# Optimization experiments

Hardware: AMD Instinct MI355X
Metric: run time of the kernel (lower is better)

The kernel has to match this reference:

```python
import jax, jax.numpy as jnp
import numpy as np

N_NODES = 50000
N_EDGES = 800000
IN_DIM = 128
HID_DIM = 128
OUT_DIM = 128
NUM_GRAPHS = 64
NUM_CLASSES = 3


def _glorot(key, shape):
    lim = np.sqrt(6.0 / (shape[0] + shape[1])).astype(np.float32)
    return jax.random.uniform(key, shape, jnp.float32, -lim, lim)


def setup_inputs() -> dict:
    key = jax.random.key(0)
    ks = jax.random.split(key, 10)
    x = jax.random.normal(ks[0], (N_NODES, IN_DIM), jnp.float32)
    edge_index = jax.random.randint(ks[1], (2, N_EDGES), 0, N_NODES, jnp.int32).astype(jnp.int64)
    batch = jnp.sort(jax.random.randint(ks[2], (N_NODES,), 0, NUM_GRAPHS, jnp.int32)).astype(jnp.int64)
    return {
        "x": x,
        "edge_index": edge_index,
        "batch": batch,
        "W1": _glorot(ks[3], (IN_DIM, HID_DIM)),  "b1": jnp.zeros((HID_DIM,), jnp.float32),
        "W2": _glorot(ks[4], (HID_DIM, HID_DIM)), "b2": jnp.zeros((HID_DIM,), jnp.float32),
        "W3": _glorot(ks[5], (HID_DIM, OUT_DIM)), "b3": jnp.zeros((OUT_DIM,), jnp.float32),
        "C1": _glorot(ks[6], (OUT_DIM, HID_DIM)), "bc1": jnp.zeros((HID_DIM,), jnp.float32),
        "C2": _glorot(ks[7], (HID_DIM, NUM_CLASSES)), "bc2": jnp.zeros((NUM_CLASSES,), jnp.float32),
    }


def _gcn_conv(x, src, dst, norm, W, b):
    # PyG GCNConv: linear transform, then normalized gather/scatter aggregation, then bias.
    h = x @ W                               # [N, F_out]
    msg = h[src] * norm[:, None]            # [E+N, F_out] irregular gather
    return jax.ops.segment_sum(msg, dst, num_segments=N_NODES) + b


def reference(x, edge_index, batch, W1, b1, W2, b2, W3, b3, C1, bc1, C2, bc2):
    loops = jnp.arange(N_NODES, dtype=edge_index.dtype)
    src = jnp.concatenate([edge_index[0], loops])  # add self-loops as in GCNConv
    dst = jnp.concatenate([edge_index[1], loops])
    deg = jax.ops.segment_sum(jnp.ones_like(dst, jnp.float32), dst, num_segments=N_NODES)
    dinv = jnp.where(deg > 0, jax.lax.rsqrt(deg), 0.0)
    norm = dinv[src] * dinv[dst]            # symmetric D^-1/2 (A+I) D^-1/2 weights

    # dropout(p=0.2) is identity at inference time
    h = jax.nn.relu(_gcn_conv(x, src, dst, norm, W1, b1))
    h = jax.nn.relu(_gcn_conv(h, src, dst, norm, W2, b2))
    h = _gcn_conv(h, src, dst, norm, W3, b3)

    # global mean pool over batch segment ids
    counts = jax.ops.segment_sum(jnp.ones((N_NODES,), jnp.float32), batch, num_segments=NUM_GRAPHS)
    pooled = jax.ops.segment_sum(h, batch, num_segments=NUM_GRAPHS) / jnp.maximum(counts, 1.0)[:, None]

    g = jax.nn.relu(pooled @ C1 + bc1)      # classifier MLP (dropout 0.3 inactive)
    return g @ C2 + bc2                     # [NUM_GRAPHS, 3]
```

## Files before the change

### kernel.cpp

```cpp
#include <hip/hip_runtime.h>
#include <hip/hip_bf16.h>

#define N_NODES    50000
#define DIM        128
#define NUM_GRAPHS 64
#define NUM_CLASSES 3
#define NPAD       50176
#define XPITCH     136

typedef unsigned short ushort_t;
typedef unsigned int   uint_t;
typedef __attribute__((ext_vector_type(8))) short short8;
typedef __attribute__((ext_vector_type(4))) float f32x4;

__device__ __forceinline__ ushort_t f2bf(float f) {
    union { float f; uint_t u; } v; v.f = f;
    uint_t r = v.u + 0x7fffu + ((v.u >> 16) & 1u);
    return (ushort_t)(r >> 16);
}
__device__ __forceinline__ float bflo(uint_t u) {
    union { uint_t u; float f; } v; v.u = u << 16; return v.f;
}
__device__ __forceinline__ float bfhi(uint_t u) {
    union { uint_t u; float f; } v; v.u = u & 0xffff0000u; return v.f;
}

__device__ __forceinline__ void gather_raw(
    int n, int lane, const int* __restrict__ rowptr,
    const int* __restrict__ csr_src, const uint_t* __restrict__ Tb,
    float2& acc)
{
    int p0 = rowptr[n], p1 = rowptr[n + 1];
    uint_t us = Tb[n * 64 + lane];
    float2 a0 = make_float2(bflo(us), bfhi(us));
    float2 a1 = make_float2(0.f, 0.f);
    int p = p0;
    int nb = (p1 - p0) >> 3;
    if (nb > 0) {
        uint_t ucur[8];
        #pragma unroll
        for (int q = 0; q < 8; ++q) ucur[q] = Tb[csr_src[p + q] * 64 + lane];
        for (int b = 1; b < nb; ++b) {
            uint_t unxt[8];
            #pragma unroll
            for (int q = 0; q < 8; ++q) unxt[q] = Tb[csr_src[p + 8 + q] * 64 + lane];
            #pragma unroll
            for (int q = 0; q < 8; q += 2) {
                a0.x += bflo(ucur[q]);     a0.y += bfhi(ucur[q]);
                a1.x += bflo(ucur[q + 1]); a1.y += bfhi(ucur[q + 1]);
            }
            #pragma unroll
            for (int q = 0; q < 8; ++q) ucur[q] = unxt[q];
            p += 8;
        }
        #pragma unroll
        for (int q = 0; q < 8; q += 2) {
            a0.x += bflo(ucur[q]);     a0.y += bfhi(ucur[q]);
            a1.x += bflo(ucur[q + 1]); a1.y += bfhi(ucur[q + 1]);
        }
        p += 8;
    }
    for (; p + 4 <= p1; p += 4) {
        int s[4]; uint_t u[4];
        #pragma unroll
        for (int q = 0; q < 4; ++q) s[q] = csr_src[p + q];
        #pragma unroll
        for (int q = 0; q < 4; ++q) u[q] = Tb[s[q] * 64 + lane];
        #pragma unroll
        for (int q = 0; q < 4; q += 2) {
            a0.x += bflo(u[q]);     a0.y += bfhi(u[q]);
            a1.x += bflo(u[q + 1]); a1.y += bfhi(u[q + 1]);
        }
    }
    for (; p < p1; ++p) {
        int s = csr_src[p];
        uint_t u = Tb[s * 64 + lane];
        a0.x += bflo(u); a0.y += bfhi(u);
    }
    acc.x += a0.x + a1.x;
    acc.y += a0.y + a1.y;
}

__global__ void k_init(int* degi, float* pooled, float* counts) {
    int i = blockIdx.x * 256 + threadIdx.x;
    if (i < NPAD) degi[i] = 0;
    if (i < NUM_GRAPHS * DIM) pooled[i] = 0.0f;
    if (i < NUM_GRAPHS) counts[i] = 0.0f;
}

__global__ void k_prep(const float* __restrict__ W1, const float* __restrict__ W2,
                       const float* __restrict__ W3, ushort_t* __restrict__ Wt) {
    int i = blockIdx.x * 256 + threadIdx.x;
    int mat = i >> 14;
    int idx = i & 16383;
    const float* W = (mat == 0) ? W1 : (mat == 1) ? W2 : W3;
    int n = idx >> 7, k = idx & 127;
    Wt[mat * 16384 + n * 128 + k] = f2bf(W[k * 128 + n]);
}

__global__ void k_count(const int* __restrict__ dst, int* degi, int* rank, int nedges) {
    int e = blockIdx.x * 256 + threadIdx.x;
    if (e < nedges) rank[e] = atomicAdd(&degi[dst[e]], 1);
}

__global__ __launch_bounds__(256) void k_scan1(const int* __restrict__ degi,
                                               int* rowptr, int* bsum) {
    __shared__ int sh[256];
    int i = blockIdx.x * 256 + threadIdx.x;
    int v = degi[i];
    sh[threadIdx.x] = v;
    __syncthreads();
    for (int off = 1; off < 256; off <<= 1) {
        int t = (threadIdx.x >= off) ? sh[threadIdx.x - off] : 0;
        __syncthreads();
        sh[threadIdx.x] += t;
        __syncthreads();
    }
    rowptr[i] = sh[threadIdx.x] - v;
    if (threadIdx.x == 255) bsum[blockIdx.x] = sh[255];
}

__global__ __launch_bounds__(256) void k_scan2(int* bsum, int nblocks) {
    __shared__ int sh[256];
    int v = (threadIdx.x < nblocks) ? bsum[threadIdx.x] : 0;
    sh[threadIdx.x] = v;
    __syncthreads();
    for (int off = 1; off < 256; off <<= 1) {
        int t = (threadIdx.x >= off) ? sh[threadIdx.x - off] : 0;
        __syncthreads();
        sh[threadIdx.x] += t;
        __syncthreads();
    }
    if (threadIdx.x < nblocks) bsum[threadIdx.x] = sh[threadIdx.x] - v;
}

__global__ __launch_bounds__(256) void k_scan3(int* rowptr, const int* __restrict__ bsum,
                                               const int* __restrict__ degi,
                                               float* dinv) {
    int i = blockIdx.x * 256 + threadIdx.x;
    rowptr[i] = rowptr[i] + bsum[blockIdx.x];
    if (i < N_NODES) dinv[i] = rsqrtf((float)degi[i] + 1.0f);
}

__global__ void k_fill(const int* __restrict__ src, const int* __restrict__ dst,
                       const int* __restrict__ rank, const int* __restrict__ rowptr,
                       int* csr_src, int nedges) {
    int e = blockIdx.x * 256 + threadIdx.x;
    if (e < nedges) csr_src[rowptr[dst[e]] + rank[e]] = src[e];
}

__global__ __launch_bounds__(256) void k_mm1(
    const float* __restrict__ xin, const ushort_t* __restrict__ WtG,
    const float* __restrict__ dinv, ushort_t* __restrict__ TbOut)
{
    __shared__ ushort_t Wl[DIM * XPITCH];
    __shared__ ushort_t Xl[64 * XPITCH];

    const int tid = threadIdx.x;
    const int rowbase = blockIdx.x * 64;

    #pragma unroll
    for (int i = 0; i < 8; ++i) {
        int g = tid + i * 256;
        uint4 v = ((const uint4*)WtG)[g];
        *((uint4*)&Wl[(g >> 4) * XPITCH + (g & 15) * 8]) = v;
    }
    #pragma unroll
    for (int i = 0; i < 8; ++i) {
        int c = tid + i * 256;
        int row = c >> 5;
        int grow = rowbase + row;
        float4 f = make_float4(0.f, 0.f, 0.f, 0.f);
        if (grow < N_NODES)
            f = ((const float4*)xin)[(long long)rowbase * 32 + c];
        ushort4 h;
        h.x = f2bf(f.x); h.y = f2bf(f.y); h.z = f2bf(f.z); h.w = f2bf(f.w);
        *((ushort4*)&Xl[row * XPITCH + (c & 31) * 4]) = h;
    }
    __syncthreads();

    const int wave = tid >> 6;
    const int lane = tid & 63;
    const int quad = lane >> 4;
    const int lm   = lane & 15;
    const int m0   = wave * 16;

    short8 af[4];
    #pragma unroll
    for (int k0 = 0; k0 < 4; ++k0)
        af[k0] = *(const short8*)&Xl[(m0 + lm) * XPITCH + k0 * 32 + quad * 8];

    int noder[4]; float di[4]; bool okr[4];
    #pragma unroll
    for (int r = 0; r < 4; ++r) {
        noder[r] = rowbase + m0 + quad * 4 + r;
        okr[r] = (noder[r] < N_NODES);
        di[r] = okr[r] ? dinv[noder[r]] : 0.f;
    }

    for (int n0 = 0; n0 < DIM; n0 += 16) {
        f32x4 acc = {0.f, 0.f, 0.f, 0.f};
        #pragma unroll
        for (int k0 = 0; k0 < 4; ++k0) {
            short8 bf = *(const short8*)&Wl[(n0 + lm) * XPITCH + k0 * 32 + quad * 8];
            acc = __builtin_amdgcn_mfma_f32_16x16x32_bf16(af[k0], bf, acc, 0, 0, 0);
        }
        int n = n0 + lm;
        #pragma unroll
        for (int r = 0; r < 4; ++r)
            if (okr[r])
                TbOut[(long long)noder[r] * DIM + n] = f2bf(acc[r] * di[r]);
    }
}

__global__ __launch_bounds__(256) void k_fused(
    const int* __restrict__ rowptr, const int* __restrict__ csr_src,
    const float* __restrict__ dinv, const uint_t* __restrict__ TbIn,
    const ushort_t* __restrict__ WtG, const float* __restrict__ b_prev,
    ushort_t* __restrict__ TbOut)
{
    __shared__ ushort_t Xl[16 * XPITCH];

    const int tid = threadIdx.x;
    const int rowbase = blockIdx.x * 16;
    const int wave = tid >> 6;
    const int lane = tid & 63;

    float2 bias2 = ((const float2*)b_prev)[lane];

    #pragma unroll
    for (int t = 0; t < 4; ++t) {
        int r = wave * 4 + t;
        int n = rowbase + r;
        float2 acc = make_float2(0.f, 0.f);
        float dd = 0.f;
        if (n < N_NODES) {
            dd = dinv[n];
            gather_raw(n, lane, rowptr, csr_src, TbIn, acc);
        }
        ushort2 h;
        h.x = f2bf(fmaxf(bias2.x + acc.x * dd, 0.f));
        h.y = f2bf(fmaxf(bias2.y + acc.y * dd, 0.f));
        *((ushort2*)&Xl[r * XPITCH + lane * 2]) = h;
    }
    __syncthreads();

    const int quad = lane >> 4;
    const int lm   = lane & 15;

    short8 af[4];
    #pragma unroll
    for (int k0 = 0; k0 < 4; ++k0)
        af[k0] = *(const short8*)&Xl[lm * XPITCH + k0 * 32 + quad * 8];

    int noder[4]; float di[4]; bool okr[4];
    #pragma unroll
    for (int r = 0; r < 4; ++r) {
        noder[r] = rowbase + quad * 4 + r;
        okr[r] = (noder[r] < N_NODES);
        di[r] = okr[r] ? dinv[noder[r]] : 0.f;
    }

    #pragma unroll
    for (int h = 0; h < 2; ++h) {
        int n0 = wave * 32 + h * 16;
        f32x4 acc = {0.f, 0.f, 0.f, 0.f};
        #pragma unroll
        for (int k0 = 0; k0 < 4; ++k0) {
            short8 bf = *(const short8*)&WtG[(n0 + lm) * DIM + k0 * 32 + quad * 8];
            acc = __builtin_amdgcn_mfma_f32_16x16x32_bf16(af[k0], bf, acc, 0, 0, 0);
        }
        int n = n0 + lm;
        #pragma unroll
        for (int r = 0; r < 4; ++r)
            if (okr[r])
                TbOut[(long long)noder[r] * DIM + n] = f2bf(acc[r] * di[r]);
    }
}

__global__ __launch_bounds__(256) void k_poolgather(
    const int* __restrict__ rowptr, const int* __restrict__ csr_src,
    const float* __restrict__ dinv, const uint_t* __restrict__ Tb,
    const float* __restrict__ b3, const int* __restrict__ batch,
    float* pooled, float* counts)
{
    __shared__ float lp[8][DIM];
    __shared__ float lc[8];

    const int tid  = threadIdx.x;
    const int wave = tid >> 6;
    const int lane = tid & 63;
    const int blk0 = blockIdx.x * 32;

    #pragma unroll
    for (int i = 0; i < 4; ++i) ((float*)lp)[tid + i * 256] = 0.f;
    if (tid < 8) lc[tid] = 0.f;
    __syncthreads();

    const int gbase = batch[min(blk0, N_NODES - 1)];
    int n0 = blk0 + wave * 8;

    if (n0 < N_NODES) {
        int nend = min(n0 + 8, N_NODES);
        float2 bias2 = ((const float2*)b3)[lane];
        int cur = batch[n0];
        int runstart = n0;
        float2 pacc = make_float2(0.f, 0.f);

        for (int n = n0; n < nend; ++n) {
            int g = batch[n];
            if (g != cur) {
                int slot = cur - gbase;
                if (slot < 8) {
                    atomicAdd(&lp[slot][2 * lane], pacc.x);
                    atomicAdd(&lp[slot][2 * lane + 1], pacc.y);
                    if (lane == 0) atomicAdd(&lc[slot], (float)(n - runstart));
                } else {
                    atomicAdd(&pooled[cur * DIM + 2 * lane], pacc.x);
                    atomicAdd(&pooled[cur * DIM + 2 * lane + 1], pacc.y);
                    if (lane == 0) atomicAdd(&counts[cur], (float)(n - runstart));
                }
                pacc.x = 0.f; pacc.y = 0.f; cur = g; runstart = n;
            }
            float2 acc = make_float2(0.f, 0.f);
            gather_raw(n, lane, rowptr, csr_src, Tb, acc);
            float dd = dinv[n];
            pacc.x += bias2.x + acc.x * dd;
            pacc.y += bias2.y + acc.y * dd;
        }
        int slot = cur - gbase;
        if (slot < 8) {
            atomicAdd(&lp[slot][2 * lane], pacc.x);
            atomicAdd(&lp[slot][2 * lane + 1], pacc.y);
            if (lane == 0) atomicAdd(&lc[slot], (float)(nend - runstart));
        } else {
            atomicAdd(&pooled[cur * DIM + 2 * lane], pacc.x);
            atomicAdd(&pooled[cur * DIM + 2 * lane + 1], pacc.y);
            if (lane == 0) atomicAdd(&counts[cur], (float)(nend - runstart));
        }
    }
    __syncthreads();

    #pragma unroll
    for (int s = 0; s < 8; ++s) {
        if (lc[s] != 0.f) {
            if (tid < DIM) atomicAdd(&pooled[(gbase + s) * DIM + tid], lp[s][tid]);
            if (tid == DIM) atomicAdd(&counts[gbase + s], lc[s]);
        }
    }
}

__global__ __launch_bounds__(128) void k_cls(
    const float* __restrict__ pooled, const float* __restrict__ counts,
    const float* __restrict__ C1, const float* __restrict__ bc1,
    const float* __restrict__ C2, const float* __restrict__ bc2,
    float* out)
{
    __shared__ float pm[DIM];
    __shared__ float gv[DIM];
    int g = blockIdx.x, j = threadIdx.x;
    float cnt = fmaxf(counts[g], 1.0f);
    pm[j] = pooled[g * DIM + j] / cnt;
    __syncthreads();
    float a = bc1[j];
    for (int k = 0; k < DIM; ++k) a += pm[k] * C1[k * DIM + j];
    gv[j] = fmaxf(a, 0.f);
    __syncthreads();
    if (j < NUM_CLASSES) {
        float o = bc2[j];
        for (int k = 0; k < DIM; ++k) o += gv[k] * C2[k * NUM_CLASSES + j];
        out[g * NUM_CLASSES + j] = o;
    }
}

extern "C" void kernel_launch(void* const* d_in, const int* in_sizes, int n_in,
                              void* d_out, int out_size, void* d_ws, size_t ws_size,
                              hipStream_t stream) {
    const float* x    = (const float*)d_in[0];
    const int*   ei   = (const int*)d_in[1];
    const int*   batch= (const int*)d_in[2];
    const float* W1   = (const float*)d_in[3];
    const float* b1   = (const float*)d_in[4];
    const float* W2   = (const float*)d_in[5];
    const float* b2   = (const float*)d_in[6];
    const float* W3   = (const float*)d_in[7];
    const float* b3   = (const float*)d_in[8];
    const float* C1   = (const float*)d_in[9];
    const float* bc1  = (const float*)d_in[10];
    const float* C2   = (const float*)d_in[11];
    const float* bc2  = (const float*)d_in[12];

    const int nedges = in_sizes[1] / 2;
    const int* src = ei;
    const int* dst = ei + nedges;

    float*    dinv    = (float*)d_ws;
    uint_t*   TbA     = (uint_t*)(dinv + NPAD);
    uint_t*   TbB     = TbA + (long long)N_NODES * 64;
    float*    pooled  = (float*)(TbB + (long long)N_NODES * 64);
    float*    counts  = pooled + NUM_GRAPHS * DIM;
    int*      degi    = (int*)(counts + 64);
    int*      rowptr  = degi + NPAD;
    int*      bsum    = rowptr + NPAD + 256;
    int*      rank    = bsum + 256;
    int*      csr_src = rank + nedges;
    ushort_t* Wt      = (ushort_t*)(csr_src + nedges);

    const int nodeBlocks = NPAD / 256;
    const int mmBlocks   = (N_NODES + 63) / 64;
    const int fusedBlocks= (N_NODES + 15) / 16;
    const int pgBlocks   = (N_NODES + 31) / 32;
    const int edgeBlocks = (nedges + 255) / 256;

    k_init<<<nodeBlocks, 256, 0, stream>>>(degi, pooled, counts);
    k_prep<<<192, 256, 0, stream>>>(W1, W2, W3, Wt);
    k_count<<<edgeBlocks, 256, 0, stream>>>(dst, degi, rank, nedges);
    k_scan1<<<nodeBlocks, 256, 0, stream>>>(degi, rowptr, bsum);
    k_scan2<<<1, 256, 0, stream>>>(bsum, nodeBlocks);
    k_scan3<<<nodeBlocks, 256, 0, stream>>>(rowptr, bsum, degi, dinv);
    k_fill<<<edgeBlocks, 256, 0, stream>>>(src, dst, rank, rowptr, csr_src, nedges);

    k_mm1<<<mmBlocks, 256, 0, stream>>>(x, Wt, dinv, (ushort_t*)TbA);
    k_fused<<<fusedBlocks, 256, 0, stream>>>(rowptr, csr_src, dinv, TbA,
                                             Wt + 16384, b1, (ushort_t*)TbB);
    k_fused<<<fusedBlocks, 256, 0, stream>>>(rowptr, csr_src, dinv, TbB,
                                             Wt + 32768, b2, (ushort_t*)TbA);
    k_poolgather<<<pgBlocks, 256, 0, stream>>>(rowptr, csr_src, dinv, TbA,
                                               b3, batch, pooled, counts);
    k_cls<<<NUM_GRAPHS, 128, 0, stream>>>(pooled, counts, C1, bc1, C2, bc2,
                                          (float*)d_out);
}
```

Baseline: 303.4 us.

## Gather neighbor rows with 16-byte loads, four edges per wave in parallel

Reworks the CSR gather so each wave splits into four 16-lane groups. Each lane loads 16 bytes (8 bf16 features) per neighbor, so one wave processes four edges per step instead of one 4-byte load per lane. Partial sums are combined with cross-lane shuffles, and the pooling kernel remaps channels to match. This is meant to raise memory-level parallelism and cut instruction count for the irregular gather, at the cost of extra shuffles, more registers and some idle lanes in the tail handling.

```diff
diff --git a/kernel.cpp b/kernel.cpp
--- a/kernel.cpp
+++ b/kernel.cpp
@@ -25,60 +25,56 @@
     union { uint_t u; float f; } v; v.u = u & 0xffff0000u; return v.f;
 }
 
-__device__ __forceinline__ void gather_raw(
-    int n, int lane, const int* __restrict__ rowptr,
-    const int* __restrict__ csr_src, const uint_t* __restrict__ Tb,
-    float2& acc)
+__device__ __forceinline__ void accum8(float* a, uint4 u) {
+    a[0] += bflo(u.x); a[1] += bfhi(u.x);
+    a[2] += bflo(u.y); a[3] += bfhi(u.y);
+    a[4] += bflo(u.z); a[5] += bfhi(u.z);
+    a[6] += bflo(u.w); a[7] += bfhi(u.w);
+}
+
+__device__ __forceinline__ void gather_x4(
+    int n, int g, int c, const int* __restrict__ rowptr,
+    const int* __restrict__ csr_src, const uint4* __restrict__ Tb4,
+    float* a)
 {
     int p0 = rowptr[n], p1 = rowptr[n + 1];
-    uint_t us = Tb[n * 64 + lane];
-    float2 a0 = make_float2(bflo(us), bfhi(us));
-    float2 a1 = make_float2(0.f, 0.f);
     int p = p0;
-    int nb = (p1 - p0) >> 3;
-    if (nb > 0) {
-        uint_t ucur[8];
-        #pragma unroll
-        for (int q = 0; q < 8; ++q) ucur[q] = Tb[csr_src[p + q] * 64 + lane];
-        for (int b = 1; b < nb; ++b) {
-            uint_t unxt[8];
+    int nb = (p1 - p0) >> 2;
+    int ng = nb >> 2;
+    if (ng > 0) {
+        uint4 cur[4];
+        int s0[4];
+        #pragma unroll
+        for (int d = 0; d < 4; ++d) s0[d] = csr_src[p + 4 * d + g];
+        #pragma unroll
+        for (int d = 0; d < 4; ++d) cur[d] = Tb4[s0[d] * 16 + c];
+        for (int b = 1; b < ng; ++b) {
+            uint4 nxt[4];
+            int s1[4];
             #pragma unroll
-            for (int q = 0; q < 8; ++q) unxt[q] = Tb[csr_src[p + 8 + q] * 64 + lane];
+            for (int d = 0; d < 4; ++d) s1[d] = csr_src[p + 16 + 4 * d + g];
             #pragma unroll
-            for (int q = 0; q < 8; q += 2) {
-                a0.x += bflo(ucur[q]);     a0.y += bfhi(ucur[q]);
-                a1.x += bflo(ucur[q + 1]); a1.y += bfhi(ucur[q + 1]);
-            }
+            for (int d = 0; d < 4; ++d) nxt[d] = Tb4[s1[d] * 16 + c];
             #pragma unroll
-            for (int q = 0; q < 8; ++q) ucur[q] = unxt[q];
-            p += 8;
-        }
-        #pragma unroll
-        for (int q = 0; q < 8; q += 2) {
-            a0.x += bflo(ucur[q]);     a0.y += bfhi(ucur[q]);
-            a1.x += bflo(ucur[q + 1]); a1.y += bfhi(ucur[q + 1]);
-        }
-        p += 8;
+            for (int d = 0; d < 4; ++d) accum8(a, cur[d]);
+            #pragma unroll
+            for (int d = 0; d < 4; ++d) cur[d] = nxt[d];
+            p += 16;
+        }
+        #pragma unroll
+        for (int d = 0; d < 4; ++d) accum8(a, cur[d]);
+        p += 16;
     }
     for (; p + 4 <= p1; p += 4) {
-        int s[4]; uint_t u[4];
-        #pragma unroll
-        for (int q = 0; q < 4; ++q) s[q] = csr_src[p + q];
-        #pragma unroll
-        for (int q = 0; q < 4; ++q) u[q] = Tb[s[q] * 64 + lane];
-        #pragma unroll
-        for (int q = 0; q < 4; q += 2) {
-            a0.x += bflo(u[q]);     a0.y += bfhi(u[q]);
-            a1.x += bflo(u[q + 1]); a1.y += bfhi(u[q + 1]);
-        }
-    }
-    for (; p < p1; ++p) {
-        int s = csr_src[p];
-        uint_t u = Tb[s * 64 + lane];
-        a0.x += bflo(u); a0.y += bfhi(u);
-    }
-    acc.x += a0.x + a1.x;
-    acc.y += a0.y + a1.y;
+        int s = csr_src[p + g];
+        uint4 u = Tb4[s * 16 + c];
+        accum8(a, u);
+    }
+    if (p + g < p1) {
+        int s = csr_src[p + g];
+        uint4 u = Tb4[s * 16 + c];
+        accum8(a, u);
+    }
 }
 
 __global__ void k_init(int* degi, float* pooled, float* counts) {
@@ -225,23 +221,43 @@
     const int rowbase = blockIdx.x * 16;
     const int wave = tid >> 6;
     const int lane = tid & 63;
-
-    float2 bias2 = ((const float2*)b_prev)[lane];
+    const int g    = lane >> 4;
+    const int c    = lane & 15;
+    const uint4* Tb4 = (const uint4*)TbIn;
+
+    float4 blo = ((const float4*)b_prev)[c * 2];
+    float4 bhi = ((const float4*)b_prev)[c * 2 + 1];
 
     #pragma unroll
     for (int t = 0; t < 4; ++t) {
         int r = wave * 4 + t;
         int n = rowbase + r;
-        float2 acc = make_float2(0.f, 0.f);
+        float a[8] = {0.f, 0.f, 0.f, 0.f, 0.f, 0.f, 0.f, 0.f};
         float dd = 0.f;
+        uint4 uself = make_uint4(0u, 0u, 0u, 0u);
         if (n < N_NODES) {
+            uself = Tb4[n * 16 + c];
             dd = dinv[n];
-            gather_raw(n, lane, rowptr, csr_src, TbIn, acc);
-        }
-        ushort2 h;
-        h.x = f2bf(fmaxf(bias2.x + acc.x * dd, 0.f));
-        h.y = f2bf(fmaxf(bias2.y + acc.y * dd, 0.f));
-        *((ushort2*)&Xl[r * XPITCH + lane * 2]) = h;
+            gather_x4(n, g, c, rowptr, csr_src, Tb4, a);
+        }
+        #pragma unroll
+        for (int i = 0; i < 8; ++i) {
+            a[i] += __shfl_xor(a[i], 16);
+            a[i] += __shfl_xor(a[i], 32);
+        }
+        accum8(a, uself);
+        if (g == 0) {
+            short8 h;
+            h[0] = (short)f2bf(fmaxf(blo.x + a[0] * dd, 0.f));
+            h[1] = (short)f2bf(fmaxf(blo.y + a[1] * dd, 0.f));
+            h[2] = (short)f2bf(fmaxf(blo.z + a[2] * dd, 0.f));
+            h[3] = (short)f2bf(fmaxf(blo.w + a[3] * dd, 0.f));
+            h[4] = (short)f2bf(fmaxf(bhi.x + a[4] * dd, 0.f));
+            h[5] = (short)f2bf(fmaxf(bhi.y + a[5] * dd, 0.f));
+            h[6] = (short)f2bf(fmaxf(bhi.z + a[6] * dd, 0.f));
+            h[7] = (short)f2bf(fmaxf(bhi.w + a[7] * dd, 0.f));
+            *((short8*)&Xl[r * XPITCH + c * 8]) = h;
+        }
     }
     __syncthreads();
 
@@ -290,7 +306,10 @@
     const int tid  = threadIdx.x;
     const int wave = tid >> 6;
     const int lane = tid & 63;
+    const int g    = lane >> 4;
+    const int c    = lane & 15;
     const int blk0 = blockIdx.x * 32;
+    const uint4* Tb4 = (const uint4*)Tb;
 
     #pragma unroll
     for (int i = 0; i < 4; ++i) ((float*)lp)[tid + i * 256] = 0.f;
@@ -299,43 +318,56 @@
 
     const int gbase = batch[min(blk0, N_NODES - 1)];
     int n0 = blk0 + wave * 8;
+    const int ch = c * 8 + 2 * g;
 
     if (n0 < N_NODES) {
         int nend = min(n0 + 8, N_NODES);
-        float2 bias2 = ((const float2*)b3)[lane];
+        float4 blo = ((const float4*)b3)[c * 2];
+        float4 bhi = ((const float4*)b3)[c * 2 + 1];
+        float bb0 = (g == 0) ? blo.x : (g == 1) ? blo.z : (g == 2) ? bhi.x : bhi.z;
+        float bb1 = (g == 0) ? blo.y : (g == 1) ? blo.w : (g == 2) ? bhi.y : bhi.w;
         int cur = batch[n0];
         int runstart = n0;
-        float2 pacc = make_float2(0.f, 0.f);
+        float pacc0 = 0.f, pacc1 = 0.f;
 
         for (int n = n0; n < nend; ++n) {
-            int g = batch[n];
-            if (g != cur) {
+            int gb = batch[n];
+            if (gb != cur) {
                 int slot = cur - gbase;
                 if (slot < 8) {
-                    atomicAdd(&lp[slot][2 * lane], pacc.x);
-                    atomicAdd(&lp[slot][2 * lane + 1], pacc.y);
+                    atomicAdd(&lp[slot][ch], pacc0);
+                    atomicAdd(&lp[slot][ch + 1], pacc1);
                     if (lane == 0) atomicAdd(&lc[slot], (float)(n - runstart));
                 } else {
-                    atomicAdd(&pooled[cur * DIM + 2 * lane], pacc.x);
-                    atomicAdd(&pooled[cur * DIM + 2 * lane + 1], pacc.y);
+                    atomicAdd(&pooled[cur * DIM + ch], pacc0);
+                    atomicAdd(&pooled[cur * DIM + ch + 1], pacc1);
                     if (lane == 0) atomicAdd(&counts[cur], (float)(n - runstart));
                 }
-                pacc.x = 0.f; pacc.y = 0.f; cur = g; runstart = n;
+                pacc0 = 0.f; pacc1 = 0.f; cur = gb; runstart = n;
             }
-            float2 acc = make_float2(0.f, 0.f);
-            gather_raw(n, lane, rowptr, csr_src, Tb, acc);
+            float a[8] = {0.f, 0.f, 0.f, 0.f, 0.f, 0.f, 0.f, 0.f};
+            uint4 uself = Tb4[n * 16 + c];
+            gather_x4(n, g, c, rowptr, csr_src, Tb4, a);
+            #pragma unroll
+            for (int i = 0; i < 8; ++i) {
+                a[i] += __shfl_xor(a[i], 16);
+                a[i] += __shfl_xor(a[i], 32);
+            }
+            accum8(a, uself);
             float dd = dinv[n];
-            pacc.x += bias2.x + acc.x * dd;
-            pacc.y += bias2.y + acc.y * dd;
+            float x0 = (g == 0) ? a[0] : (g == 1) ? a[2] : (g == 2) ? a[4] : a[6];
+            float x1 = (g == 0) ? a[1] : (g == 1) ? a[3] : (g == 2) ? a[5] : a[7];
+            pacc0 += bb0 + x0 * dd;
+            pacc1 += bb1 + x1 * dd;
         }
         int slot = cur - gbase;
         if (slot < 8) {
-            atomicAdd(&lp[slot][2 * lane], pacc.x);
-            atomicAdd(&lp[slot][2 * lane + 1], pacc.y);
+            atomicAdd(&lp[slot][ch], pacc0);
+            atomicAdd(&lp[slot][ch + 1], pacc1);
             if (lane == 0) atomicAdd(&lc[slot], (float)(nend - runstart));
         } else {
-            atomicAdd(&pooled[cur * DIM + 2 * lane], pacc.x);
-            atomicAdd(&pooled[cur * DIM + 2 * lane + 1], pacc.y);
+            atomicAdd(&pooled[cur * DIM + ch], pacc0);
+            atomicAdd(&pooled[cur * DIM + ch + 1], pacc1);
             if (lane == 0) atomicAdd(&counts[cur], (float)(nend - runstart));
         }
     }
```

Result: slower. 334.6 us (+10.3%).

## Replace final-layer gather and pooling with precomputed per-graph weighted reduction

Applied to the files above, without the earlier changes.

Mean pooling is linear, so pooling the last GCN aggregation can be rewritten as a weighted sum of the transformed features. A dense per-graph weight matrix (64 x NPAD) is precomputed with atomics over edges and self-loops. A new kernel then reduces each graph's weight row against the bf16 features, loading only rows whose weight is non-zero. The bias is added after the mean in the classifier, and node counts now come from the weight-building kernel. This removes the CSR gather over all edges in the last layer. In exchange it adds a 12.8 MB zero-fill, a pass of scattered float atomics and a dense scan of that matrix, while each source row is still loaded once per distinct graph it feeds into.

```diff
diff --git a/kernel.cpp b/kernel.cpp
--- a/kernel.cpp
+++ b/kernel.cpp
@@ -88,6 +88,11 @@
     if (i < NUM_GRAPHS) counts[i] = 0.0f;
 }
 
+__global__ void k_init_wgs(float* Wgs) {
+    int i = blockIdx.x * 256 + threadIdx.x;
+    ((float4*)Wgs)[i] = make_float4(0.f, 0.f, 0.f, 0.f);
+}
+
 __global__ void k_prep(const float* __restrict__ W1, const float* __restrict__ W2,
                        const float* __restrict__ W3, ushort_t* __restrict__ Wt) {
     int i = blockIdx.x * 256 + threadIdx.x;
@@ -147,6 +152,34 @@
                        int* csr_src, int nedges) {
     int e = blockIdx.x * 256 + threadIdx.x;
     if (e < nedges) csr_src[rowptr[dst[e]] + rank[e]] = src[e];
+}
+
+__global__ void k_wgs_e(const int* __restrict__ src, const int* __restrict__ dst,
+                        const int* __restrict__ batch, const float* __restrict__ dinv,
+                        float* Wgs, int nedges) {
+    int e = blockIdx.x * 256 + threadIdx.x;
+    if (e < nedges) {
+        int n = dst[e];
+        int g = batch[n];
+        atomicAdd(&Wgs[g * NPAD + src[e]], dinv[n]);
+    }
+}
+
+__global__ __launch_bounds__(256) void k_wgs_n(const int* __restrict__ batch,
+                                               const float* __restrict__ dinv,
+                                               float* Wgs, float* counts) {
+    __shared__ float lh[NUM_GRAPHS];
+    int tid = threadIdx.x;
+    int i = blockIdx.x * 256 + tid;
+    if (tid < NUM_GRAPHS) lh[tid] = 0.f;
+    __syncthreads();
+    if (i < N_NODES) {
+        int g = batch[i];
+        atomicAdd(&Wgs[g * NPAD + i], dinv[i]);
+        atomicAdd(&lh[g], 1.0f);
+    }
+    __syncthreads();
+    if (tid < NUM_GRAPHS && lh[tid] != 0.f) atomicAdd(&counts[tid], lh[tid]);
 }
 
 __global__ __launch_bounds__(256) void k_mm1(
@@ -278,80 +311,54 @@
     }
 }
 
-__global__ __launch_bounds__(256) void k_poolgather(
-    const int* __restrict__ rowptr, const int* __restrict__ csr_src,
-    const float* __restrict__ dinv, const uint_t* __restrict__ Tb,
-    const float* __restrict__ b3, const int* __restrict__ batch,
-    float* pooled, float* counts)
+__global__ __launch_bounds__(256) void k_poolmm(
+    const float* __restrict__ Wgs, const uint_t* __restrict__ Y,
+    float* pooled)
 {
-    __shared__ float lp[8][DIM];
-    __shared__ float lc[8];
+    __shared__ float lsum[DIM];
 
     const int tid  = threadIdx.x;
     const int wave = tid >> 6;
     const int lane = tid & 63;
-    const int blk0 = blockIdx.x * 32;
-
-    #pragma unroll
-    for (int i = 0; i < 4; ++i) ((float*)lp)[tid + i * 256] = 0.f;
-    if (tid < 8) lc[tid] = 0.f;
-    __syncthreads();
-
-    const int gbase = batch[min(blk0, N_NODES - 1)];
-    int n0 = blk0 + wave * 8;
-
-    if (n0 < N_NODES) {
-        int nend = min(n0 + 8, N_NODES);
-        float2 bias2 = ((const float2*)b3)[lane];
-        int cur = batch[n0];
-        int runstart = n0;
-        float2 pacc = make_float2(0.f, 0.f);
-
-        for (int n = n0; n < nend; ++n) {
-            int g = batch[n];
-            if (g != cur) {
-                int slot = cur - gbase;
-                if (slot < 8) {
-                    atomicAdd(&lp[slot][2 * lane], pacc.x);
-                    atomicAdd(&lp[slot][2 * lane + 1], pacc.y);
-                    if (lane == 0) atomicAdd(&lc[slot], (float)(n - runstart));
-                } else {
-                    atomicAdd(&pooled[cur * DIM + 2 * lane], pacc.x);
-                    atomicAdd(&pooled[cur * DIM + 2 * lane + 1], pacc.y);
-                    if (lane == 0) atomicAdd(&counts[cur], (float)(n - runstart));
-                }
-                pacc.x = 0.f; pacc.y = 0.f; cur = g; runstart = n;
-            }
-            float2 acc = make_float2(0.f, 0.f);
-            gather_raw(n, lane, rowptr, csr_src, Tb, acc);
-            float dd = dinv[n];
-            pacc.x += bias2.x + acc.x * dd;
-            pacc.y += bias2.y + acc.y * dd;
-        }
-        int slot = cur - gbase;
-        if (slot < 8) {
-            atomicAdd(&lp[slot][2 * lane], pacc.x);
-            atomicAdd(&lp[slot][2 * lane + 1], pacc.y);
-            if (lane == 0) atomicAdd(&lc[slot], (float)(nend - runstart));
-        } else {
-            atomicAdd(&pooled[cur * DIM + 2 * lane], pacc.x);
-            atomicAdd(&pooled[cur * DIM + 2 * lane + 1], pacc.y);
-            if (lane == 0) atomicAdd(&counts[cur], (float)(nend - runstart));
-        }
-    }
-    __syncthreads();
-
-    #pragma unroll
-    for (int s = 0; s < 8; ++s) {
-        if (lc[s] != 0.f) {
-            if (tid < DIM) atomicAdd(&pooled[(gbase + s) * DIM + tid], lp[s][tid]);
-            if (tid == DIM) atomicAdd(&counts[gbase + s], lc[s]);
-        }
-    }
+    const int g    = blockIdx.x;
+    const int s0   = blockIdx.y * 1024 + wave * 256;
+
+    if (tid < DIM) lsum[tid] = 0.f;
+    __syncthreads();
+
+    const float* wrow = Wgs + g * NPAD + s0;
+    float2 acc = make_float2(0.f, 0.f);
+
+    for (int i0 = 0; i0 < 256; i0 += 16) {
+        float4 w0 = *(const float4*)(wrow + i0);
+        float4 w1 = *(const float4*)(wrow + i0 + 4);
+        float4 w2 = *(const float4*)(wrow + i0 + 8);
+        float4 w3 = *(const float4*)(wrow + i0 + 12);
+        float w[16] = {w0.x, w0.y, w0.z, w0.w, w1.x, w1.y, w1.z, w1.w,
+                       w2.x, w2.y, w2.z, w2.w, w3.x, w3.y, w3.z, w3.w};
+        uint_t u[16];
+        #pragma unroll
+        for (int q = 0; q < 16; ++q) {
+            u[q] = 0u;
+            if (w[q] != 0.f) u[q] = Y[(s0 + i0 + q) * 64 + lane];
+        }
+        #pragma unroll
+        for (int q = 0; q < 16; ++q) {
+            acc.x += w[q] * bflo(u[q]);
+            acc.y += w[q] * bfhi(u[q]);
+        }
+    }
+
+    atomicAdd(&lsum[2 * lane], acc.x);
+    atomicAdd(&lsum[2 * lane + 1], acc.y);
+    __syncthreads();
+    if (tid < DIM && lsum[tid] != 0.f)
+        atomicAdd(&pooled[g * DIM + tid], lsum[tid]);
 }
 
 __global__ __launch_bounds__(128) void k_cls(
     const float* __restrict__ pooled, const float* __restrict__ counts,
+    const float* __restrict__ b3,
     const float* __restrict__ C1, const float* __restrict__ bc1,
     const float* __restrict__ C2, const float* __restrict__ bc2,
     float* out)
@@ -360,7 +367,7 @@
     __shared__ float gv[DIM];
     int g = blockIdx.x, j = threadIdx.x;
     float cnt = fmaxf(counts[g], 1.0f);
-    pm[j] = pooled[g * DIM + j] / cnt;
+    pm[j] = pooled[g * DIM + j] / cnt + b3[j];
     __syncthreads();
     float a = bc1[j];
     for (int k = 0; k < DIM; ++k) a += pm[k] * C1[k * DIM + j];
@@ -405,28 +412,31 @@
     int*      rank    = bsum + 256;
     int*      csr_src = rank + nedges;
     ushort_t* Wt      = (ushort_t*)(csr_src + nedges);
+    float*    Wgs     = (float*)(Wt + 3 * 16384);
 
     const int nodeBlocks = NPAD / 256;
     const int mmBlocks   = (N_NODES + 63) / 64;
     const int fusedBlocks= (N_NODES + 15) / 16;
-    const int pgBlocks   = (N_NODES + 31) / 32;
     const int edgeBlocks = (nedges + 255) / 256;
+    const int wgsBlocks  = NUM_GRAPHS * NPAD / 4 / 256;
 
     k_init<<<nodeBlocks, 256, 0, stream>>>(degi, pooled, counts);
+    k_init_wgs<<<wgsBlocks, 256, 0, stream>>>(Wgs);
     k_prep<<<192, 256, 0, stream>>>(W1, W2, W3, Wt);
     k_count<<<edgeBlocks, 256, 0, stream>>>(dst, degi, rank, nedges);
     k_scan1<<<nodeBlocks, 256, 0, stream>>>(degi, rowptr, bsum);
     k_scan2<<<1, 256, 0, stream>>>(bsum, nodeBlocks);
     k_scan3<<<nodeBlocks, 256, 0, stream>>>(rowptr, bsum, degi, dinv);
     k_fill<<<edgeBlocks, 256, 0, stream>>>(src, dst, rank, rowptr, csr_src, nedges);
+    k_wgs_e<<<edgeBlocks, 256, 0, stream>>>(src, dst, batch, dinv, Wgs, nedges);
+    k_wgs_n<<<nodeBlocks, 256, 0, stream>>>(batch, dinv, Wgs, counts);
 
     k_mm1<<<mmBlocks, 256, 0, stream>>>(x, Wt, dinv, (ushort_t*)TbA);
     k_fused<<<fusedBlocks, 256, 0, stream>>>(rowptr, csr_src, dinv, TbA,
                                              Wt + 16384, b1, (ushort_t*)TbB);
     k_fused<<<fusedBlocks, 256, 0, stream>>>(rowptr, csr_src, dinv, TbB,
                                              Wt + 32768, b2, (ushort_t*)TbA);
-    k_poolgather<<<pgBlocks, 256, 0, stream>>>(rowptr, csr_src, dinv, TbA,
-                                               b3, batch, pooled, counts);
-    k_cls<<<NUM_GRAPHS, 128, 0, stream>>>(pooled, counts, C1, bc1, C2, bc2,
+    k_poolmm<<<dim3(NUM_GRAPHS, NPAD / 1024), 256, 0, stream>>>(Wgs, TbA, pooled);
+    k_cls<<<NUM_GRAPHS, 128, 0, stream>>>(pooled, counts, b3, C1, bc1, C2, bc2,
                                           (float*)d_out);
 }
```

After: 358.4 us. 18.1% more time.
